# Kernel tuning notes

Hardware: AMD Instinct MI355X
Metric: run time of the kernel (lower is better)

The kernel has to match this reference:

```python
import jax, jax.numpy as jnp
import numpy as np

N = 50000      # current-level nodes
N_NEXT = 2000  # next-level nodes
E = 1600000    # directed edges (before self-loops)
D_IN = 128
D_OUT = 128
LN_EPS = 1e-5


def setup_inputs() -> dict:
    key = jax.random.key(0)
    ks = jax.random.split(key, 12)
    curr_h = jax.random.normal(ks[0], (N, D_IN), dtype=jnp.float32)
    next_h = jax.random.normal(ks[1], (N_NEXT, D_IN), dtype=jnp.float32)
    inc = jax.random.uniform(ks[2], (N, N_NEXT), dtype=jnp.float32)
    src = jax.random.randint(ks[3], (E,), 0, N, dtype=jnp.int64)
    dst = jax.random.randint(ks[4], (E,), 0, N, dtype=jnp.int64)
    s = 1.0 / np.sqrt(D_IN)
    W_conv = jax.random.normal(ks[5], (D_IN, D_OUT), dtype=jnp.float32) * s
    b_conv = jnp.zeros((D_OUT,), dtype=jnp.float32)
    W_fus = jax.random.normal(ks[6], (D_IN, D_OUT), dtype=jnp.float32) * s
    b_fus = jnp.zeros((D_OUT,), dtype=jnp.float32)
    conv_w = jax.random.uniform(ks[7], (D_OUT,), dtype=jnp.float32)
    topDown_w = jax.random.uniform(ks[8], (D_OUT,), dtype=jnp.float32)
    ln_gamma = jnp.ones((D_OUT,), dtype=jnp.float32)
    ln_beta = jnp.zeros((D_OUT,), dtype=jnp.float32)
    return {
        "curr_h": curr_h, "next_h": next_h, "inc": inc,
        "src": src, "dst": dst,
        "W_conv": W_conv, "b_conv": b_conv,
        "W_fus": W_fus, "b_fus": b_fus,
        "conv_w": conv_w, "topDown_w": topDown_w,
        "ln_gamma": ln_gamma, "ln_beta": ln_beta,
    }


def _graph_conv(x, W, b, src_sl, dst_sl, norm_out, norm_in):
    # DGL GraphConv, norm='both': D_out^{-1/2} on src, sum-aggregate, D_in^{-1/2} on dst.
    h = x @ W                               # [N, D_OUT]
    h = h * norm_out[:, None]
    agg = jax.ops.segment_sum(h[src_sl], dst_sl, num_segments=N)  # SpMM
    return agg * norm_in[:, None] + b


def reference(curr_h, next_h, inc, src, dst,
              W_conv, b_conv, W_fus, b_fus,
              conv_w, topDown_w, ln_gamma, ln_beta):
    # dgl.add_self_loop
    loop = jnp.arange(N, dtype=src.dtype)
    src_sl = jnp.concatenate([src, loop])
    dst_sl = jnp.concatenate([dst, loop])
    ones = jnp.ones_like(src_sl, dtype=jnp.float32)
    out_deg = jax.ops.segment_sum(ones, src_sl, num_segments=N)
    in_deg = jax.ops.segment_sum(ones, dst_sl, num_segments=N)
    norm_out = jax.lax.rsqrt(out_deg)  # >=1 due to self-loops
    norm_in = jax.lax.rsqrt(in_deg)

    conv_layer = _graph_conv(curr_h, W_conv, b_conv, src_sl, dst_sl, norm_out, norm_in) * conv_w[None, :]
    fused_in = inc @ next_h  # dense incidence matmul [N, D_IN]
    top_down = _graph_conv(fused_in, W_fus, b_fus, src_sl, dst_sl, norm_out, norm_in) * topDown_w[None, :]

    result = conv_layer + top_down
    # LayerNorm over last dim
    mu = jnp.mean(result, axis=-1, keepdims=True)
    var = jnp.mean((result - mu) ** 2, axis=-1, keepdims=True)
    result = (result - mu) * jax.lax.rsqrt(var + LN_EPS) * ln_gamma + ln_beta
    # dropout p=0.0 (eval) -> identity; activation ReLU
    return jax.nn.relu(result)
```

## Files before the change

kernel.cpp:

```cpp
#include <hip/hip_runtime.h>
#include <hip/hip_bf16.h>

#define N_NODES   50000
#define EDGES     1600000
#define D         128
#define K_INC     2000
#define K_TOT     2128
#define K_PAD     2176
#define LN_EPS    1e-5f

typedef float f32x4 __attribute__((ext_vector_type(4)));
typedef short short8 __attribute__((ext_vector_type(8)));

__global__ void probe_kernel(const int* __restrict__ src, int* __restrict__ flag) {
    __shared__ int any_nonzero;
    if (threadIdx.x == 0) any_nonzero = 0;
    __syncthreads();
    int v = src[threadIdx.x * 2 + 1];
    if (v != 0) any_nonzero = 1;
    __syncthreads();
    if (threadIdx.x == 0) flag[0] = any_nonzero ? 0 : 1;
}

__global__ void zero_kernel(int* __restrict__ p, int n) {
    int i = blockIdx.x * 256 + threadIdx.x;
    if (i < n) p[i] = 0;
}

__global__ void deg_kernel(const int* __restrict__ src, const int* __restrict__ dst,
                           const int* __restrict__ flag,
                           int* __restrict__ out_deg, int* __restrict__ in_cnt) {
    int e = blockIdx.x * 256 + threadIdx.x;
    int st = 1 + flag[0];
    if (e < EDGES) {
        atomicAdd(&out_deg[src[e * st]], 1);
        atomicAdd(&in_cnt[dst[e * st]], 1);
    }
}

__global__ __launch_bounds__(1024) void scan_kernel(const int* __restrict__ cnt,
                                                    int* __restrict__ row_start) {
    __shared__ int buf[1024];
    int t = threadIdx.x;
    const int N = N_NODES;
    int chunk = (N + 1023) / 1024;
    int lo = t * chunk, hi = min(lo + chunk, N);
    int s = 0;
    for (int i = lo; i < hi; ++i) s += cnt[i];
    buf[t] = s;
    __syncthreads();
    for (int off = 1; off < 1024; off <<= 1) {
        int v = (t >= off) ? buf[t - off] : 0;
        __syncthreads();
        buf[t] += v;
        __syncthreads();
    }
    int run = (t > 0) ? buf[t - 1] : 0;
    for (int i = lo; i < hi; ++i) { row_start[i] = run; run += cnt[i]; }
    if (t == 1023) row_start[N] = buf[1023];
}

__global__ void fill_kernel(const int* __restrict__ src, const int* __restrict__ dst,
                            const int* __restrict__ flag,
                            const int* __restrict__ row_start, int* __restrict__ cursor,
                            int* __restrict__ csr_src) {
    int e = blockIdx.x * 256 + threadIdx.x;
    int st = 1 + flag[0];
    if (e < EDGES) {
        int d = dst[e * st];
        int pos = atomicAdd(&cursor[d], 1);
        csr_src[row_start[d] + pos] = src[e * st];
    }
}

__global__ __launch_bounds__(128) void p_kernel(
    const float* __restrict__ next_h, const float* __restrict__ W_fus,
    const float* __restrict__ topDown_w, const float* __restrict__ W_conv,
    const float* __restrict__ conv_w, __hip_bfloat16* __restrict__ PbT) {
    int k = blockIdx.x, n = threadIdx.x;
    float v;
    if (k < K_INC) {
        __shared__ float nh[D];
        nh[n] = next_h[k * D + n];
        __syncthreads();
        float acc = 0.f;
        for (int j = 0; j < D; ++j) acc += nh[j] * W_fus[j * D + n];
        v = acc * topDown_w[n];
    } else if (k < K_TOT) {
        v = W_conv[(k - K_INC) * D + n] * conv_w[n];
    } else {
        v = 0.f;
    }
    PbT[(size_t)n * K_PAD + k] = __float2bfloat16(v);
}

__global__ __launch_bounds__(256) void gemm_kernel(
    const float* __restrict__ inc, const float* __restrict__ curr_h,
    const ushort* __restrict__ PbT, const int* __restrict__ out_deg,
    float* __restrict__ Zs) {
    __shared__ ushort As[128][40];
    __shared__ ushort Bs[128][40];
    const int N = N_NODES;
    int tid = threadIdx.x;
    int wave = tid >> 6, lane = tid & 63;
    int wm = wave >> 1, wn = wave & 1;
    int r = lane & 15, q = lane >> 4;
    int rowBase = blockIdx.x * 128;

    f32x4 acc[4][4] = {};

    for (int kt = 0; kt < K_PAD / 32; ++kt) {
        int k0 = kt * 32;
        __syncthreads();
#pragma unroll
        for (int it = 0; it < 4; ++it) {
            int id = tid + it * 256;
            int arow = id >> 3, q4 = id & 7;
            int gk = k0 + q4 * 4;
            int grow = rowBase + arow; if (grow >= N) grow = N - 1;
            float4 va;
            if (gk < K_INC)      va = *(const float4*)(inc + (size_t)grow * K_INC + gk);
            else if (gk < K_TOT) va = *(const float4*)(curr_h + (size_t)grow * D + (gk - K_INC));
            else                 va = make_float4(0.f, 0.f, 0.f, 0.f);
            ushort4 hb;
            hb.x = __hip_bfloat16_raw(__float2bfloat16(va.x)).x;
            hb.y = __hip_bfloat16_raw(__float2bfloat16(va.y)).x;
            hb.z = __hip_bfloat16_raw(__float2bfloat16(va.z)).x;
            hb.w = __hip_bfloat16_raw(__float2bfloat16(va.w)).x;
            *(ushort4*)&As[arow][q4 * 4] = hb;
        }
#pragma unroll
        for (int it = 0; it < 2; ++it) {
            int id = tid + it * 256;
            int brow = id >> 2, qc = id & 3;
            uint4 vb = *(const uint4*)(PbT + (size_t)brow * K_PAD + k0 + qc * 8);
            *(uint4*)&Bs[brow][qc * 8] = vb;
        }
        __syncthreads();
        short8 af[4], bfr[4];
#pragma unroll
        for (int mi = 0; mi < 4; ++mi) af[mi] = *(const short8*)&As[wm * 64 + mi * 16 + r][q * 8];
#pragma unroll
        for (int ni = 0; ni < 4; ++ni) bfr[ni] = *(const short8*)&Bs[wn * 64 + ni * 16 + r][q * 8];
#pragma unroll
        for (int mi = 0; mi < 4; ++mi)
#pragma unroll
            for (int ni = 0; ni < 4; ++ni)
                acc[mi][ni] = __builtin_amdgcn_mfma_f32_16x16x32_bf16(af[mi], bfr[ni], acc[mi][ni], 0, 0, 0);
    }

#pragma unroll
    for (int mi = 0; mi < 4; ++mi) {
#pragma unroll
        for (int j = 0; j < 4; ++j) {
            int grow = rowBase + wm * 64 + mi * 16 + q * 4 + j;
            if (grow < N) {
                float no = rsqrtf((float)(out_deg[grow] + 1));
#pragma unroll
                for (int ni = 0; ni < 4; ++ni) {
                    int col = wn * 64 + ni * 16 + r;
                    Zs[(size_t)grow * D + col] = acc[mi][ni][j] * no;
                }
            }
        }
    }
}

__global__ __launch_bounds__(128) void agg_ln_kernel(
    const float* __restrict__ Zs, const int* __restrict__ row_start,
    const int* __restrict__ csr_src,
    const float* __restrict__ b_conv, const float* __restrict__ b_fus,
    const float* __restrict__ conv_w, const float* __restrict__ topDown_w,
    const float* __restrict__ gamma, const float* __restrict__ beta,
    float* __restrict__ out) {
    int i = blockIdx.x, c = threadIdx.x;
    float acc = Zs[(size_t)i * D + c];
    int beg = row_start[i], end = row_start[i + 1];
    for (int e = beg; e < end; ++e) {
        int s = csr_src[e];
        acc += Zs[(size_t)s * D + c];
    }
    float norm_in = rsqrtf((float)(end - beg + 1));
    float cv = b_conv[c] * conv_w[c] + b_fus[c] * topDown_w[c];
    float y = acc * norm_in + cv;

    float s1 = y, s2 = y * y;
#pragma unroll
    for (int off = 32; off > 0; off >>= 1) {
        s1 += __shfl_down(s1, off);
        s2 += __shfl_down(s2, off);
    }
    __shared__ float sh[4];
    int wid = threadIdx.x >> 6;
    if ((threadIdx.x & 63) == 0) { sh[wid * 2] = s1; sh[wid * 2 + 1] = s2; }
    __syncthreads();
    float S = sh[0] + sh[2], SS = sh[1] + sh[3];
    float mu = S * (1.f / D);
    float var = SS * (1.f / D) - mu * mu;
    float rstd = rsqrtf(var + LN_EPS);
    float rv = (y - mu) * rstd * gamma[c] + beta[c];
    out[(size_t)i * D + c] = fmaxf(rv, 0.f);
}

extern "C" void kernel_launch(void* const* d_in, const int* in_sizes, int n_in,
                              void* d_out, int out_size, void* d_ws, size_t ws_size,
                              hipStream_t stream) {
    const float* curr_h    = (const float*)d_in[0];
    const float* next_h    = (const float*)d_in[1];
    const float* inc       = (const float*)d_in[2];
    const int*   src       = (const int*)d_in[3];
    const int*   dst       = (const int*)d_in[4];
    const float* W_conv    = (const float*)d_in[5];
    const float* b_conv    = (const float*)d_in[6];
    const float* W_fus     = (const float*)d_in[7];
    const float* b_fus     = (const float*)d_in[8];
    const float* conv_w    = (const float*)d_in[9];
    const float* topDown_w = (const float*)d_in[10];
    const float* ln_gamma  = (const float*)d_in[11];
    const float* ln_beta   = (const float*)d_in[12];

    const int N = N_NODES;
    const int E = EDGES;

    char* p = (char*)d_ws;
    float* Zs = (float*)p;                    p += (size_t)N * D * sizeof(float);
    __hip_bfloat16* PbT = (__hip_bfloat16*)p; p += (size_t)D * K_PAD * 2;
    int* out_deg   = (int*)p;                 p += (size_t)N * 4;
    int* in_cnt    = (int*)p;                 p += (size_t)N * 4;
    int* cursor    = (int*)p;                 p += (size_t)N * 4;
    int* row_start = (int*)p;                 p += (size_t)(N + 1) * 4;
    int* idx_flag  = (int*)p;                 p += 256;
    int* csr_src   = (int*)p;                 p += (size_t)E * 4;

    probe_kernel<<<1, 1024, 0, stream>>>(src, idx_flag);
    zero_kernel<<<(3 * N + 255) / 256, 256, 0, stream>>>(out_deg, 3 * N);
    deg_kernel<<<(E + 255) / 256, 256, 0, stream>>>(src, dst, idx_flag, out_deg, in_cnt);
    scan_kernel<<<1, 1024, 0, stream>>>(in_cnt, row_start);
    fill_kernel<<<(E + 255) / 256, 256, 0, stream>>>(src, dst, idx_flag, row_start, cursor, csr_src);
    p_kernel<<<K_PAD, 128, 0, stream>>>(next_h, W_fus, topDown_w, W_conv, conv_w, PbT);
    gemm_kernel<<<(N + 127) / 128, 256, 0, stream>>>(inc, curr_h, (const ushort*)PbT, out_deg, Zs);
    agg_ln_kernel<<<N, 128, 0, stream>>>(Zs, row_start, csr_src,
                                         b_conv, b_fus, conv_w, topDown_w,
                                         ln_gamma, ln_beta, (float*)d_out);
}
```

Before: 1.116 ms.

## Store intermediate Zs in bf16, retile GEMM, warp-per-node aggregation

```diff
diff --git a/kernel.cpp b/kernel.cpp
--- a/kernel.cpp
+++ b/kernel.cpp
@@ -11,6 +11,12 @@
 
 typedef float f32x4 __attribute__((ext_vector_type(4)));
 typedef short short8 __attribute__((ext_vector_type(8)));
+
+__device__ __forceinline__ ushort f2bf(float x) {
+    return __hip_bfloat16_raw(__float2bfloat16(x)).x;
+}
+__device__ __forceinline__ float bf_lo(uint v) { return __uint_as_float(v << 16); }
+__device__ __forceinline__ float bf_hi(uint v) { return __uint_as_float(v & 0xffff0000u); }
 
 __global__ void probe_kernel(const int* __restrict__ src, int* __restrict__ flag) {
     __shared__ int any_nonzero;
@@ -76,7 +82,7 @@
 __global__ __launch_bounds__(128) void p_kernel(
     const float* __restrict__ next_h, const float* __restrict__ W_fus,
     const float* __restrict__ topDown_w, const float* __restrict__ W_conv,
-    const float* __restrict__ conv_w, __hip_bfloat16* __restrict__ PbT) {
+    const float* __restrict__ conv_w, ushort* __restrict__ PbT) {
     int k = blockIdx.x, n = threadIdx.x;
     float v;
     if (k < K_INC) {
@@ -91,115 +97,127 @@
     } else {
         v = 0.f;
     }
-    PbT[(size_t)n * K_PAD + k] = __float2bfloat16(v);
+    PbT[(size_t)n * K_PAD + k] = f2bf(v);
 }
 
 __global__ __launch_bounds__(256) void gemm_kernel(
     const float* __restrict__ inc, const float* __restrict__ curr_h,
     const ushort* __restrict__ PbT, const int* __restrict__ out_deg,
-    float* __restrict__ Zs) {
-    __shared__ ushort As[128][40];
-    __shared__ ushort Bs[128][40];
+    ushort* __restrict__ Zs) {
+    __shared__ ushort As[64][72];
+    __shared__ ushort Bs[128][72];
     const int N = N_NODES;
     int tid = threadIdx.x;
     int wave = tid >> 6, lane = tid & 63;
     int wm = wave >> 1, wn = wave & 1;
     int r = lane & 15, q = lane >> 4;
-    int rowBase = blockIdx.x * 128;
-
-    f32x4 acc[4][4] = {};
-
-    for (int kt = 0; kt < K_PAD / 32; ++kt) {
-        int k0 = kt * 32;
+    int rowBase = blockIdx.x * 64;
+
+    f32x4 acc[2][4] = {};
+
+    for (int kt = 0; kt < K_PAD / 64; ++kt) {
+        int k0 = kt * 64;
         __syncthreads();
 #pragma unroll
         for (int it = 0; it < 4; ++it) {
             int id = tid + it * 256;
-            int arow = id >> 3, q4 = id & 7;
-            int gk = k0 + q4 * 4;
+            int arow = id >> 4, c4 = id & 15;
+            int gk = k0 + c4 * 4;
             int grow = rowBase + arow; if (grow >= N) grow = N - 1;
             float4 va;
             if (gk < K_INC)      va = *(const float4*)(inc + (size_t)grow * K_INC + gk);
             else if (gk < K_TOT) va = *(const float4*)(curr_h + (size_t)grow * D + (gk - K_INC));
             else                 va = make_float4(0.f, 0.f, 0.f, 0.f);
             ushort4 hb;
-            hb.x = __hip_bfloat16_raw(__float2bfloat16(va.x)).x;
-            hb.y = __hip_bfloat16_raw(__float2bfloat16(va.y)).x;
-            hb.z = __hip_bfloat16_raw(__float2bfloat16(va.z)).x;
-            hb.w = __hip_bfloat16_raw(__float2bfloat16(va.w)).x;
-            *(ushort4*)&As[arow][q4 * 4] = hb;
-        }
-#pragma unroll
-        for (int it = 0; it < 2; ++it) {
+            hb.x = f2bf(va.x); hb.y = f2bf(va.y); hb.z = f2bf(va.z); hb.w = f2bf(va.w);
+            *(ushort4*)&As[arow][c4 * 4] = hb;
+        }
+#pragma unroll
+        for (int it = 0; it < 4; ++it) {
             int id = tid + it * 256;
-            int brow = id >> 2, qc = id & 3;
-            uint4 vb = *(const uint4*)(PbT + (size_t)brow * K_PAD + k0 + qc * 8);
-            *(uint4*)&Bs[brow][qc * 8] = vb;
-        }
-        __syncthreads();
-        short8 af[4], bfr[4];
-#pragma unroll
-        for (int mi = 0; mi < 4; ++mi) af[mi] = *(const short8*)&As[wm * 64 + mi * 16 + r][q * 8];
-#pragma unroll
-        for (int ni = 0; ni < 4; ++ni) bfr[ni] = *(const short8*)&Bs[wn * 64 + ni * 16 + r][q * 8];
-#pragma unroll
-        for (int mi = 0; mi < 4; ++mi)
+            int brow = id >> 3, c8 = id & 7;
+            uint4 vb = *(const uint4*)(PbT + (size_t)brow * K_PAD + k0 + c8 * 8);
+            *(uint4*)&Bs[brow][c8 * 8] = vb;
+        }
+        __syncthreads();
+#pragma unroll
+        for (int kk = 0; kk < 2; ++kk) {
+            short8 af[2], bfr[4];
+#pragma unroll
+            for (int mi = 0; mi < 2; ++mi)
+                af[mi] = *(const short8*)&As[wm * 32 + mi * 16 + r][kk * 32 + q * 8];
 #pragma unroll
             for (int ni = 0; ni < 4; ++ni)
-                acc[mi][ni] = __builtin_amdgcn_mfma_f32_16x16x32_bf16(af[mi], bfr[ni], acc[mi][ni], 0, 0, 0);
-    }
-
-#pragma unroll
-    for (int mi = 0; mi < 4; ++mi) {
+                bfr[ni] = *(const short8*)&Bs[wn * 64 + ni * 16 + r][kk * 32 + q * 8];
+#pragma unroll
+            for (int mi = 0; mi < 2; ++mi)
+#pragma unroll
+                for (int ni = 0; ni < 4; ++ni)
+                    acc[mi][ni] = __builtin_amdgcn_mfma_f32_16x16x32_bf16(af[mi], bfr[ni], acc[mi][ni], 0, 0, 0);
+        }
+    }
+
+#pragma unroll
+    for (int mi = 0; mi < 2; ++mi) {
 #pragma unroll
         for (int j = 0; j < 4; ++j) {
-            int grow = rowBase + wm * 64 + mi * 16 + q * 4 + j;
+            int grow = rowBase + wm * 32 + mi * 16 + q * 4 + j;
             if (grow < N) {
                 float no = rsqrtf((float)(out_deg[grow] + 1));
 #pragma unroll
                 for (int ni = 0; ni < 4; ++ni) {
                     int col = wn * 64 + ni * 16 + r;
-                    Zs[(size_t)grow * D + col] = acc[mi][ni][j] * no;
+                    Zs[(size_t)grow * D + col] = f2bf(acc[mi][ni][j] * no);
                 }
             }
         }
     }
 }
 
-__global__ __launch_bounds__(128) void agg_ln_kernel(
-    const float* __restrict__ Zs, const int* __restrict__ row_start,
+__global__ __launch_bounds__(256) void agg_ln_kernel(
+    const ushort* __restrict__ Zs, const int* __restrict__ row_start,
     const int* __restrict__ csr_src,
     const float* __restrict__ b_conv, const float* __restrict__ b_fus,
     const float* __restrict__ conv_w, const float* __restrict__ topDown_w,
     const float* __restrict__ gamma, const float* __restrict__ beta,
     float* __restrict__ out) {
-    int i = blockIdx.x, c = threadIdx.x;
-    float acc = Zs[(size_t)i * D + c];
-    int beg = row_start[i], end = row_start[i + 1];
-    for (int e = beg; e < end; ++e) {
-        int s = csr_src[e];
-        acc += Zs[(size_t)s * D + c];
-    }
-    float norm_in = rsqrtf((float)(end - beg + 1));
-    float cv = b_conv[c] * conv_w[c] + b_fus[c] * topDown_w[c];
-    float y = acc * norm_in + cv;
-
-    float s1 = y, s2 = y * y;
-#pragma unroll
-    for (int off = 32; off > 0; off >>= 1) {
-        s1 += __shfl_down(s1, off);
-        s2 += __shfl_down(s2, off);
-    }
-    __shared__ float sh[4];
-    int wid = threadIdx.x >> 6;
-    if ((threadIdx.x & 63) == 0) { sh[wid * 2] = s1; sh[wid * 2 + 1] = s2; }
-    __syncthreads();
-    float S = sh[0] + sh[2], SS = sh[1] + sh[3];
-    float mu = S * (1.f / D);
-    float var = SS * (1.f / D) - mu * mu;
+    int wid = threadIdx.x >> 6, lane = threadIdx.x & 63;
+    int node = blockIdx.x * 4 + wid;
+    if (node >= N_NODES) return;
+    int c0 = lane * 2;
+
+    uint v = *(const uint*)(Zs + (size_t)node * D + c0);
+    float a0 = bf_lo(v), a1 = bf_hi(v);
+    int beg = row_start[node], end = row_start[node + 1];
+    int e = beg;
+    for (; e + 1 < end; e += 2) {
+        int s0 = csr_src[e], s1 = csr_src[e + 1];
+        uint v0 = *(const uint*)(Zs + (size_t)s0 * D + c0);
+        uint v1 = *(const uint*)(Zs + (size_t)s1 * D + c0);
+        a0 += bf_lo(v0) + bf_lo(v1);
+        a1 += bf_hi(v0) + bf_hi(v1);
+    }
+    if (e < end) {
+        int s0 = csr_src[e];
+        uint v0 = *(const uint*)(Zs + (size_t)s0 * D + c0);
+        a0 += bf_lo(v0); a1 += bf_hi(v0);
+    }
+    float nin = rsqrtf((float)(end - beg + 1));
+    float y0 = a0 * nin + b_conv[c0] * conv_w[c0] + b_fus[c0] * topDown_w[c0];
+    float y1 = a1 * nin + b_conv[c0 + 1] * conv_w[c0 + 1] + b_fus[c0 + 1] * topDown_w[c0 + 1];
+
+    float s1v = y0 + y1, s2v = y0 * y0 + y1 * y1;
+#pragma unroll
+    for (int off = 1; off < 64; off <<= 1) {
+        s1v += __shfl_xor(s1v, off);
+        s2v += __shfl_xor(s2v, off);
+    }
+    float mu = s1v * (1.f / D);
+    float var = s2v * (1.f / D) - mu * mu;
     float rstd = rsqrtf(var + LN_EPS);
-    float rv = (y - mu) * rstd * gamma[c] + beta[c];
-    out[(size_t)i * D + c] = fmaxf(rv, 0.f);
+    float r0 = (y0 - mu) * rstd * gamma[c0] + beta[c0];
+    float r1 = (y1 - mu) * rstd * gamma[c0 + 1] + beta[c0 + 1];
+    *(float2*)(out + (size_t)node * D + c0) = make_float2(fmaxf(r0, 0.f), fmaxf(r1, 0.f));
 }
 
 extern "C" void kernel_launch(void* const* d_in, const int* in_sizes, int n_in,
@@ -223,14 +241,14 @@
     const int E = EDGES;
 
     char* p = (char*)d_ws;
-    float* Zs = (float*)p;                    p += (size_t)N * D * sizeof(float);
-    __hip_bfloat16* PbT = (__hip_bfloat16*)p; p += (size_t)D * K_PAD * 2;
-    int* out_deg   = (int*)p;                 p += (size_t)N * 4;
-    int* in_cnt    = (int*)p;                 p += (size_t)N * 4;
-    int* cursor    = (int*)p;                 p += (size_t)N * 4;
-    int* row_start = (int*)p;                 p += (size_t)(N + 1) * 4;
-    int* idx_flag  = (int*)p;                 p += 256;
-    int* csr_src   = (int*)p;                 p += (size_t)E * 4;
+    ushort* Zs = (ushort*)p;     p += (size_t)N * D * sizeof(ushort);
+    ushort* PbT = (ushort*)p;    p += (size_t)D * K_PAD * 2;
+    int* out_deg   = (int*)p;    p += (size_t)N * 4;
+    int* in_cnt    = (int*)p;    p += (size_t)N * 4;
+    int* cursor    = (int*)p;    p += (size_t)N * 4;
+    int* row_start = (int*)p;    p += (size_t)(N + 1) * 4;
+    int* idx_flag  = (int*)p;    p += 256;
+    int* csr_src   = (int*)p;    p += (size_t)E * 4;
 
     probe_kernel<<<1, 1024, 0, stream>>>(src, idx_flag);
     zero_kernel<<<(3 * N + 255) / 256, 256, 0, stream>>>(out_deg, 3 * N);
@@ -238,8 +256,8 @@
     scan_kernel<<<1, 1024, 0, stream>>>(in_cnt, row_start);
     fill_kernel<<<(E + 255) / 256, 256, 0, stream>>>(src, dst, idx_flag, row_start, cursor, csr_src);
     p_kernel<<<K_PAD, 128, 0, stream>>>(next_h, W_fus, topDown_w, W_conv, conv_w, PbT);
-    gemm_kernel<<<(N + 127) / 128, 256, 0, stream>>>(inc, curr_h, (const ushort*)PbT, out_deg, Zs);
-    agg_ln_kernel<<<N, 128, 0, stream>>>(Zs, row_start, csr_src,
-                                         b_conv, b_fus, conv_w, topDown_w,
-                                         ln_gamma, ln_beta, (float*)d_out);
-}
+    gemm_kernel<<<(N + 63) / 64, 256, 0, stream>>>(inc, curr_h, PbT, out_deg, Zs);
+    agg_ln_kernel<<<(N + 3) / 4, 256, 0, stream>>>(Zs, row_start, csr_src,
+                                                   b_conv, b_fus, conv_w, topDown_w,
+                                                   ln_gamma, ln_beta, (float*)d_out);
+}
```

After: 982.6 us. 1.14x faster.
